# Optimization experiments

Measured on AMD Instinct MI355X. Metric: run time of the kernel, lower is better.

The kernel has to match this reference:

```python
import jax, jax.numpy as jnp
import numpy as np
from math import atanh

B, T, D_IN, H = 16, 1024, 512, 1024
INIT_A = atanh(0.95)


def setup_inputs() -> dict:
    key = jax.random.key(0)
    k1, k2, k3, k4 = jax.random.split(key, 4)
    x = jax.random.normal(k1, (B, T, D_IN), dtype=jnp.float32)
    h0 = jax.random.normal(k2, (B, H), dtype=jnp.float32)
    # raw_a initialized near atanh(0.95) as in the module, with small jitter
    raw_a = INIT_A + 0.01 * jax.random.normal(k3, (H,), dtype=jnp.float32)
    # xavier-uniform for W_x.weight [H, D_IN]
    limit = float(np.sqrt(6.0 / (D_IN + H)))
    W = jax.random.uniform(k4, (H, D_IN), dtype=jnp.float32, minval=-limit, maxval=limit)
    b = jnp.zeros((H,), dtype=jnp.float32)
    return {"x": x, "h0": h0, "raw_a": raw_a, "W": W, "b": b}


def reference(x, h0, raw_a, W, b):
    # h_t = a * h_{t-1} + W x_t + b, computed via cumprod/cumsum parallel-scan trick
    a = jnp.tanh(raw_a)                                   # [H] (rho is None)
    z = jnp.einsum('btd,hd->bth', x, W) + b               # [B,T,H]
    A = jnp.broadcast_to(a, (x.shape[1], a.shape[0]))     # [T,H]
    p = jnp.cumprod(A, axis=0)[None]                      # [1,T,H], p[t] = a^(t+1)
    v = jnp.cumsum(z / jnp.maximum(p, 1e-12), axis=1)     # [B,T,H]
    h = v * p + p * h0[:, None, :]                        # include initial state
    zero_mask = (jnp.abs(a) < 1e-6)[None, None, :]        # degenerate a ~ 0 channels
    h = jnp.where(zero_mask, z, h)
    return h
```

## Files before the change

kernel.cpp:

```cpp
#include <hip/hip_runtime.h>
#include <cstdint>

#define B_DIM 16
#define T_DIM 1024
#define DK    512
#define H_DIM 1024

typedef __bf16 bf16x8 __attribute__((ext_vector_type(8)));
typedef __bf16 bf16x4 __attribute__((ext_vector_type(4)));
typedef float  f32x4  __attribute__((ext_vector_type(4)));

typedef __attribute__((address_space(1))) unsigned int* as1p;
typedef __attribute__((address_space(3))) unsigned int* as3p;

__device__ __forceinline__ void async_cp16(const void* g, void* l) {
  __builtin_amdgcn_global_load_lds((as1p)(uint64_t)g,
                                   (as3p)(uint32_t)(uint64_t)l, 16, 0, 0);
}

__global__ __launch_bounds__(256) void cvt_f32_bf16(const float* __restrict__ in,
                                                    __bf16* __restrict__ out, int n4) {
  int i = blockIdx.x * 256 + threadIdx.x;
  if (i >= n4) return;
  f32x4 v = ((const f32x4*)in)[i];
  bf16x4 o;
  o.x = (__bf16)v.x; o.y = (__bf16)v.y; o.z = (__bf16)v.z; o.w = (__bf16)v.w;
  ((bf16x4*)out)[i] = o;
}

__global__ __launch_bounds__(256) void compute_meta(const float* __restrict__ raw_a,
                                                    float4* __restrict__ meta) {
  int h = blockIdx.x * 256 + threadIdx.x;
  if (h >= H_DIM) return;
  float a = tanhf(raw_a[h]);
  float la2 = log2f(fabsf(a));
  meta[h] = make_float4(a, la2, (a < 0.f) ? 1.f : 0.f, (fabsf(a) < 1e-6f) ? 1.f : 0.f);
}

__global__ __launch_bounds__(256, 2) void fused_rnn(const __bf16* __restrict__ xb,
                                                    const __bf16* __restrict__ wb,
                                                    const float* __restrict__ bias,
                                                    const float4* __restrict__ meta,
                                                    const float* __restrict__ h0g,
                                                    float* __restrict__ out) {
  __shared__ __align__(16) __bf16 As[2][2][256][32];
  __shared__ __align__(16) __bf16 Bs[2][2][32][32];
  __shared__ float chunkTot[4][32];
  __shared__ float colCarry[32];

  const int tid  = threadIdx.x;
  const int wave = tid >> 6;
  const int lane = tid & 63;
  const int q = lane >> 4;
  const int c = lane & 15;

  const int b  = blockIdx.x & 15;
  const int n0 = (blockIdx.x >> 4) * 32;

  float bias_j[2], la2_j[2], h0_j[2];
  bool neg_j[2], zm_j[2];
#pragma unroll
  for (int j = 0; j < 2; ++j) {
    const int col = n0 + j * 16 + c;
    bias_j[j] = bias[col];
    const float4 mt = meta[col];
    la2_j[j] = mt.y;
    neg_j[j] = mt.z != 0.f;
    zm_j[j]  = mt.w != 0.f;
    h0_j[j]  = h0g[(size_t)b * H_DIM + col];
  }

  if (tid < 32) colCarry[tid] = 0.f;

  const int srow = lane >> 2;
  const int skof = (lane & 3) * 8;

  const __bf16* const xbB = xb + (size_t)b * T_DIM * DK;

  auto stage = [&](int t0, int k0, int buf) {
#pragma unroll
    for (int h = 0; h < 2; ++h) {
#pragma unroll
      for (int r = 0; r < 4; ++r) {
        const int rg = wave * 64 + r * 16;
        const __bf16* ga = xbB + (size_t)(t0 + rg + srow) * DK + k0 + h * 32 + skof;
        async_cp16(ga, &As[buf][h][rg][0]);
      }
    }
    {
      const int h = wave >> 1, rp = (wave & 1) * 16;
      const __bf16* gb = wb + (size_t)(n0 + rp + srow) * DK + k0 + (wave >> 1) * 32 + skof;
      async_cp16(gb, &Bs[buf][h][rp][0]);
    }
  };

  stage(0, 0, 0);
  __syncthreads();

  for (int mc = 0; mc < 4; ++mc) {
    const int t0 = mc * 256;

    f32x4 acc[4][2];
#pragma unroll
    for (int i = 0; i < 4; ++i)
#pragma unroll
      for (int j = 0; j < 2; ++j) acc[i][j] = (f32x4){0.f, 0.f, 0.f, 0.f};

    for (int k = 0; k < 8; ++k) {
      const int buf = k & 1;
      if (k < 7)       stage(t0, (k + 1) * 64, buf ^ 1);
      else if (mc < 3) stage(t0 + 256, 0, 0);
#pragma unroll
      for (int ks = 0; ks < 2; ++ks) {
        bf16x8 af[4], bfr[2];
#pragma unroll
        for (int i = 0; i < 4; ++i)
          af[i] = *(const bf16x8*)(&As[buf][ks][wave * 64 + i * 16 + c][q * 8]);
#pragma unroll
        for (int j = 0; j < 2; ++j)
          bfr[j] = *(const bf16x8*)(&Bs[buf][ks][j * 16 + c][q * 8]);
#pragma unroll
        for (int i = 0; i < 4; ++i)
#pragma unroll
          for (int j = 0; j < 2; ++j)
            acc[i][j] = __builtin_amdgcn_mfma_f32_16x16x32_bf16(af[i], bfr[j], acc[i][j], 0, 0, 0);
      }
      __syncthreads();
    }

    f32x4 vloc[4][2];
    float icarry[2] = {0.f, 0.f};
#pragma unroll
    for (int i = 0; i < 4; ++i) {
#pragma unroll
      for (int j = 0; j < 2; ++j) {
        const float la2 = la2_j[j];
        f32x4 w;
#pragma unroll
        for (int r = 0; r < 4; ++r) {
          const int tp1 = t0 + wave * 64 + i * 16 + q * 4 + r + 1;
          const float z = acc[i][j][r] + bias_j[j];
          float inv = fminf(__builtin_amdgcn_exp2f(-la2 * (float)tp1), 1e12f);
          if (neg_j[j] && (tp1 & 1)) inv = 1e12f;
          w[r] = z * inv;
        }
        const float pr0 = w[0];
        const float pr1 = pr0 + w[1];
        const float pr2 = pr1 + w[2];
        const float pr3 = pr2 + w[3];
        const float x1 = __shfl_xor(pr3, 16, 64);
        const float x2 = __shfl_xor(pr3, 32, 64);
        const float x3 = __shfl_xor(pr3, 48, 64);
        float sq = 0.f;
        if (q >= 2) sq += x2 + x3;
        if (q & 1) sq += x1;
        const float base = icarry[j] + sq;
        vloc[i][j] = (f32x4){base + pr0, base + pr1, base + pr2, base + pr3};
        icarry[j] += pr3 + x1 + x2 + x3;
      }
    }
    if (q == 0) {
#pragma unroll
      for (int j = 0; j < 2; ++j) chunkTot[wave][j * 16 + c] = icarry[j];
    }
    __syncthreads();

    float cc[2];
#pragma unroll
    for (int j = 0; j < 2; ++j) {
      float s = colCarry[j * 16 + c];
      for (int w2 = 0; w2 < 4; ++w2)
        if (w2 < wave) s += chunkTot[w2][j * 16 + c];
      cc[j] = s;
    }
#pragma unroll
    for (int i = 0; i < 4; ++i) {
#pragma unroll
      for (int j = 0; j < 2; ++j) {
        const float la2 = la2_j[j];
        const int col = n0 + j * 16 + c;
#pragma unroll
        for (int r = 0; r < 4; ++r) {
          const int tl = t0 + wave * 64 + i * 16 + q * 4 + r;
          const int tp1 = tl + 1;
          float pv = __builtin_amdgcn_exp2f(la2 * (float)tp1);
          if (neg_j[j] && (tp1 & 1)) pv = -pv;
          const float v = cc[j] + vloc[i][j][r];
          const float hv = pv * v + pv * h0_j[j];
          const float zval = acc[i][j][r] + bias_j[j];
          out[(size_t)(b * T_DIM + tl) * H_DIM + col] = zm_j[j] ? zval : hv;
        }
      }
    }
    __syncthreads();
    if (tid < 32)
      colCarry[tid] += chunkTot[0][tid] + chunkTot[1][tid] + chunkTot[2][tid] + chunkTot[3][tid];
  }
}

extern "C" void kernel_launch(void* const* d_in, const int* in_sizes, int n_in,
                              void* d_out, int out_size, void* d_ws, size_t ws_size,
                              hipStream_t stream) {
  const float* x     = (const float*)d_in[0];
  const float* h0    = (const float*)d_in[1];
  const float* raw_a = (const float*)d_in[2];
  const float* W     = (const float*)d_in[3];
  const float* bias  = (const float*)d_in[4];
  float* out = (float*)d_out;

  char* ws = (char*)d_ws;
  __bf16* xb   = (__bf16*)(ws);
  __bf16* wb   = (__bf16*)(ws + 16777216);
  float4* meta = (float4*)(ws + 16777216 + 1048576);

  cvt_f32_bf16<<<(B_DIM * T_DIM * DK / 4 + 255) / 256, 256, 0, stream>>>(x, xb, B_DIM * T_DIM * DK / 4);
  cvt_f32_bf16<<<(H_DIM * DK / 4 + 255) / 256, 256, 0, stream>>>(W, wb, H_DIM * DK / 4);
  compute_meta<<<H_DIM / 256, 256, 0, stream>>>(raw_a, meta);
  fused_rnn<<<512, 256, 0, stream>>>(xb, wb, bias, meta, h0, out);
}
```

Measured before the change: 137.4 us.

## Split time into chunks across blocks with flag-based decoupled carry propagation

The fused kernel now splits the time axis into 128-step chunks handled by separate blocks. Each block has 512 threads and covers a 64-column strip, giving 2048 blocks instead of 512. Chunk carries pass between blocks through global flag words that are polled with atomics, replacing the serial in-block loop over four 256-step chunks. W is stored transposed and preloaded whole into LDS, while x is read straight from global memory into registers. The three prep kernels merge into one launch that also zeroes the flags. The cross-block spin-wait assumes earlier chunks get scheduled, which risks stalls or a deadlock if blocks run out of order.

```diff
diff --git a/kernel.cpp b/kernel.cpp
--- a/kernel.cpp
+++ b/kernel.cpp
@@ -6,6 +6,12 @@
 #define DK    512
 #define H_DIM 1024
 
+#define TCH    128
+#define NCH    (T_DIM / TCH)
+#define NB     64
+#define NSTRIP (H_DIM / NB)
+#define NKQ    (DK / 8)
+
 typedef __bf16 bf16x8 __attribute__((ext_vector_type(8)));
 typedef __bf16 bf16x4 __attribute__((ext_vector_type(4)));
 typedef float  f32x4  __attribute__((ext_vector_type(4)));
@@ -18,50 +24,79 @@
                                    (as3p)(uint32_t)(uint64_t)l, 16, 0, 0);
 }
 
-__global__ __launch_bounds__(256) void cvt_f32_bf16(const float* __restrict__ in,
-                                                    __bf16* __restrict__ out, int n4) {
-  int i = blockIdx.x * 256 + threadIdx.x;
-  if (i >= n4) return;
-  f32x4 v = ((const f32x4*)in)[i];
-  bf16x4 o;
-  o.x = (__bf16)v.x; o.y = (__bf16)v.y; o.z = (__bf16)v.z; o.w = (__bf16)v.w;
-  ((bf16x4*)out)[i] = o;
-}
-
-__global__ __launch_bounds__(256) void compute_meta(const float* __restrict__ raw_a,
-                                                    float4* __restrict__ meta) {
-  int h = blockIdx.x * 256 + threadIdx.x;
-  if (h >= H_DIM) return;
-  float a = tanhf(raw_a[h]);
-  float la2 = log2f(fabsf(a));
-  meta[h] = make_float4(a, la2, (a < 0.f) ? 1.f : 0.f, (fabsf(a) < 1e-6f) ? 1.f : 0.f);
-}
-
-__global__ __launch_bounds__(256, 2) void fused_rnn(const __bf16* __restrict__ xb,
-                                                    const __bf16* __restrict__ wb,
-                                                    const float* __restrict__ bias,
-                                                    const float4* __restrict__ meta,
-                                                    const float* __restrict__ h0g,
-                                                    float* __restrict__ out) {
-  __shared__ __align__(16) __bf16 As[2][2][256][32];
-  __shared__ __align__(16) __bf16 Bs[2][2][32][32];
-  __shared__ float chunkTot[4][32];
-  __shared__ float colCarry[32];
+__global__ __launch_bounds__(256) void prep(const float* __restrict__ x,
+                                            __bf16* __restrict__ xb,
+                                            const float* __restrict__ W,
+                                            __bf16* __restrict__ wbT,
+                                            const float* __restrict__ raw_a,
+                                            float4* __restrict__ meta,
+                                            unsigned long long* __restrict__ flags) {
+  const int bid = blockIdx.x, tid = threadIdx.x;
+  if (bid < 8192) {
+    const int i = bid * 256 + tid;
+    f32x4 v = ((const f32x4*)x)[i];
+    bf16x4 o;
+    o.x = (__bf16)v.x; o.y = (__bf16)v.y; o.z = (__bf16)v.z; o.w = (__bf16)v.w;
+    ((bf16x4*)xb)[i] = o;
+  } else if (bid < 8704) {
+    const int i = (bid - 8192) * 256 + tid;
+    const int h  = i >> 7;
+    const int k0 = (i & 127) * 4;
+    f32x4 v = ((const f32x4*)W)[i];
+    bf16x4 o;
+    o.x = (__bf16)v.x; o.y = (__bf16)v.y; o.z = (__bf16)v.z; o.w = (__bf16)v.w;
+    *(bf16x4*)(wbT + ((size_t)(k0 >> 3) * H_DIM + h) * 8 + (k0 & 7)) = o;
+  } else if (bid < 8708) {
+    const int h = (bid - 8704) * 256 + tid;
+    const float a = tanhf(raw_a[h]);
+    const float la2 = log2f(fabsf(a));
+    meta[h] = make_float4(a, la2, (a < 0.f) ? 1.f : 0.f, (fabsf(a) < 1e-6f) ? 1.f : 0.f);
+  } else {
+    const int i = (bid - 8708) * 256 + tid;
+    flags[i] = 0ULL;
+  }
+}
+
+__global__ __launch_bounds__(512, 4) void fused_rnn(
+    const __bf16* __restrict__ xb,
+    const __bf16* __restrict__ wbT,
+    const float* __restrict__ bias,
+    const float4* __restrict__ meta,
+    const float* __restrict__ h0g,
+    unsigned long long* __restrict__ flags,
+    float* __restrict__ out) {
+  __shared__ __align__(16) __bf16 Bs[NKQ][NB][8];
+  __shared__ float chunkTot[4][NB];
+  __shared__ float colCarry[NB];
 
   const int tid  = threadIdx.x;
   const int wave = tid >> 6;
   const int lane = tid & 63;
-  const int q = lane >> 4;
-  const int c = lane & 15;
-
-  const int b  = blockIdx.x & 15;
-  const int n0 = (blockIdx.x >> 4) * 32;
+  const int q  = lane >> 4;
+  const int c  = lane & 15;
+  const int rw = wave & 3;
+  const int cg = wave >> 2;
+
+  const int bid   = blockIdx.x;
+  const int g     = bid & 127;
+  const int strip = bid >> 7;
+  const int b     = g >> 3;
+  const int chunk = g & 7;
+  const int t0    = chunk * TCH;
+  const int n0    = strip * NB;
+
+#pragma unroll
+  for (int it = 0; it < 8; ++it) {
+    const int idx = it * 512 + tid;
+    const int col = idx & 63, kq = idx >> 6;
+    async_cp16(wbT + ((size_t)kq * H_DIM + (n0 + col)) * 8, &Bs[kq][col][0]);
+  }
 
   float bias_j[2], la2_j[2], h0_j[2];
   bool neg_j[2], zm_j[2];
 #pragma unroll
   for (int j = 0; j < 2; ++j) {
-    const int col = n0 + j * 16 + c;
+    const int col = n0 + cg * 32 + j * 16 + c;
     bias_j[j] = bias[col];
     const float4 mt = meta[col];
     la2_j[j] = mt.y;
@@ -70,131 +105,118 @@
     h0_j[j]  = h0g[(size_t)b * H_DIM + col];
   }
 
-  if (tid < 32) colCarry[tid] = 0.f;
-
-  const int srow = lane >> 2;
-  const int skof = (lane & 3) * 8;
-
-  const __bf16* const xbB = xb + (size_t)b * T_DIM * DK;
-
-  auto stage = [&](int t0, int k0, int buf) {
-#pragma unroll
-    for (int h = 0; h < 2; ++h) {
+  const __bf16* const arow =
+      xb + ((size_t)(b * T_DIM + t0 + rw * 32 + c)) * DK + q * 8;
+
+  f32x4 acc[2][2];
+#pragma unroll
+  for (int i = 0; i < 2; ++i)
+#pragma unroll
+    for (int j = 0; j < 2; ++j) acc[i][j] = (f32x4){0.f, 0.f, 0.f, 0.f};
+
+  __syncthreads();
+
+#pragma unroll 4
+  for (int k = 0; k < 16; ++k) {
+    bf16x8 af[2], bfr[2];
+#pragma unroll
+    for (int i = 0; i < 2; ++i)
+      af[i] = *(const bf16x8*)(arow + (size_t)i * 16 * DK + k * 32);
+#pragma unroll
+    for (int j = 0; j < 2; ++j)
+      bfr[j] = *(const bf16x8*)(&Bs[k * 4 + q][cg * 32 + j * 16 + c][0]);
+#pragma unroll
+    for (int i = 0; i < 2; ++i)
+#pragma unroll
+      for (int j = 0; j < 2; ++j)
+        acc[i][j] = __builtin_amdgcn_mfma_f32_16x16x32_bf16(af[i], bfr[j], acc[i][j], 0, 0, 0);
+  }
+
+  f32x4 vloc[2][2];
+  float icarry[2] = {0.f, 0.f};
+#pragma unroll
+  for (int i = 0; i < 2; ++i) {
+#pragma unroll
+    for (int j = 0; j < 2; ++j) {
+      const float la2 = la2_j[j];
+      f32x4 w;
 #pragma unroll
       for (int r = 0; r < 4; ++r) {
-        const int rg = wave * 64 + r * 16;
-        const __bf16* ga = xbB + (size_t)(t0 + rg + srow) * DK + k0 + h * 32 + skof;
-        async_cp16(ga, &As[buf][h][rg][0]);
+        const int tp1 = t0 + rw * 32 + i * 16 + q * 4 + r + 1;
+        const float z = acc[i][j][r] + bias_j[j];
+        float inv = fminf(__builtin_amdgcn_exp2f(-la2 * (float)tp1), 1e12f);
+        if (neg_j[j] && (tp1 & 1)) inv = 1e12f;
+        w[r] = z * inv;
+      }
+      const float pr0 = w[0];
+      const float pr1 = pr0 + w[1];
+      const float pr2 = pr1 + w[2];
+      const float pr3 = pr2 + w[3];
+      const float x1 = __shfl_xor(pr3, 16, 64);
+      const float x2 = __shfl_xor(pr3, 32, 64);
+      const float x3 = __shfl_xor(pr3, 48, 64);
+      float sq = 0.f;
+      if (q >= 2) sq += x2 + x3;
+      if (q & 1) sq += x1;
+      const float base = icarry[j] + sq;
+      vloc[i][j] = (f32x4){base + pr0, base + pr1, base + pr2, base + pr3};
+      icarry[j] += pr3 + x1 + x2 + x3;
+    }
+  }
+  if (q == 0) {
+#pragma unroll
+    for (int j = 0; j < 2; ++j) chunkTot[rw][cg * 32 + j * 16 + c] = icarry[j];
+  }
+  __syncthreads();
+
+  if (tid < 64) {
+    const int col = tid;
+    const size_t fb = ((size_t)b * NSTRIP + strip) * NCH * NB;
+    const float tot =
+        chunkTot[0][col] + chunkTot[1][col] + chunkTot[2][col] + chunkTot[3][col];
+    atomicExch(&flags[fb + (size_t)chunk * NB + col],
+               (1ULL << 32) | (unsigned long long)__float_as_uint(tot));
+    float s = 0.f;
+    for (int p = 0; p < chunk; ++p) {
+      unsigned long long v = atomicAdd(&flags[fb + (size_t)p * NB + col], 0ULL);
+      while (!(v >> 32)) {
+        __builtin_amdgcn_s_sleep(4);
+        v = atomicAdd(&flags[fb + (size_t)p * NB + col], 0ULL);
+      }
+      s += __uint_as_float((unsigned int)v);
+    }
+    colCarry[col] = s;
+  }
+  __syncthreads();
+
+  float cc[2];
+#pragma unroll
+  for (int j = 0; j < 2; ++j) {
+    const int colL = cg * 32 + j * 16 + c;
+    float s = colCarry[colL];
+#pragma unroll
+    for (int w2 = 0; w2 < 3; ++w2)
+      if (w2 < rw) s += chunkTot[w2][colL];
+    cc[j] = s;
+  }
+#pragma unroll
+  for (int i = 0; i < 2; ++i) {
+#pragma unroll
+    for (int j = 0; j < 2; ++j) {
+      const float la2 = la2_j[j];
+      const int col = n0 + cg * 32 + j * 16 + c;
+#pragma unroll
+      for (int r = 0; r < 4; ++r) {
+        const int tl = t0 + rw * 32 + i * 16 + q * 4 + r;
+        const int tp1 = tl + 1;
+        float pv = __builtin_amdgcn_exp2f(la2 * (float)tp1);
+        if (neg_j[j] && (tp1 & 1)) pv = -pv;
+        const float v = cc[j] + vloc[i][j][r];
+        const float hv = pv * v + pv * h0_j[j];
+        const float zval = acc[i][j][r] + bias_j[j];
+        out[(size_t)(b * T_DIM + tl) * H_DIM + col] = zm_j[j] ? zval : hv;
       }
     }
-    {
-      const int h = wave >> 1, rp = (wave & 1) * 16;
-      const __bf16* gb = wb + (size_t)(n0 + rp + srow) * DK + k0 + (wave >> 1) * 32 + skof;
-      async_cp16(gb, &Bs[buf][h][rp][0]);
-    }
-  };
-
-  stage(0, 0, 0);
-  __syncthreads();
-
-  for (int mc = 0; mc < 4; ++mc) {
-    const int t0 = mc * 256;
-
-    f32x4 acc[4][2];
-#pragma unroll
-    for (int i = 0; i < 4; ++i)
-#pragma unroll
-      for (int j = 0; j < 2; ++j) acc[i][j] = (f32x4){0.f, 0.f, 0.f, 0.f};
-
-    for (int k = 0; k < 8; ++k) {
-      const int buf = k & 1;
-      if (k < 7)       stage(t0, (k + 1) * 64, buf ^ 1);
-      else if (mc < 3) stage(t0 + 256, 0, 0);
-#pragma unroll
-      for (int ks = 0; ks < 2; ++ks) {
-        bf16x8 af[4], bfr[2];
-#pragma unroll
-        for (int i = 0; i < 4; ++i)
-          af[i] = *(const bf16x8*)(&As[buf][ks][wave * 64 + i * 16 + c][q * 8]);
-#pragma unroll
-        for (int j = 0; j < 2; ++j)
-          bfr[j] = *(const bf16x8*)(&Bs[buf][ks][j * 16 + c][q * 8]);
-#pragma unroll
-        for (int i = 0; i < 4; ++i)
-#pragma unroll
-          for (int j = 0; j < 2; ++j)
-            acc[i][j] = __builtin_amdgcn_mfma_f32_16x16x32_bf16(af[i], bfr[j], acc[i][j], 0, 0, 0);
-      }
-      __syncthreads();
-    }
-
-    f32x4 vloc[4][2];
-    float icarry[2] = {0.f, 0.f};
-#pragma unroll
-    for (int i = 0; i < 4; ++i) {
-#pragma unroll
-      for (int j = 0; j < 2; ++j) {
-        const float la2 = la2_j[j];
-        f32x4 w;
-#pragma unroll
-        for (int r = 0; r < 4; ++r) {
-          const int tp1 = t0 + wave * 64 + i * 16 + q * 4 + r + 1;
-          const float z = acc[i][j][r] + bias_j[j];
-          float inv = fminf(__builtin_amdgcn_exp2f(-la2 * (float)tp1), 1e12f);
-          if (neg_j[j] && (tp1 & 1)) inv = 1e12f;
-          w[r] = z * inv;
-        }
-        const float pr0 = w[0];
-        const float pr1 = pr0 + w[1];
-        const float pr2 = pr1 + w[2];
-        const float pr3 = pr2 + w[3];
-        const float x1 = __shfl_xor(pr3, 16, 64);
-        const float x2 = __shfl_xor(pr3, 32, 64);
-        const float x3 = __shfl_xor(pr3, 48, 64);
-        float sq = 0.f;
-        if (q >= 2) sq += x2 + x3;
-        if (q & 1) sq += x1;
-        const float base = icarry[j] + sq;
-        vloc[i][j] = (f32x4){base + pr0, base + pr1, base + pr2, base + pr3};
-        icarry[j] += pr3 + x1 + x2 + x3;
-      }
-    }
-    if (q == 0) {
-#pragma unroll
-      for (int j = 0; j < 2; ++j) chunkTot[wave][j * 16 + c] = icarry[j];
-    }
-    __syncthreads();
-
-    float cc[2];
-#pragma unroll
-    for (int j = 0; j < 2; ++j) {
-      float s = colCarry[j * 16 + c];
-      for (int w2 = 0; w2 < 4; ++w2)
-        if (w2 < wave) s += chunkTot[w2][j * 16 + c];
-      cc[j] = s;
-    }
-#pragma unroll
-    for (int i = 0; i < 4; ++i) {
-#pragma unroll
-      for (int j = 0; j < 2; ++j) {
-        const float la2 = la2_j[j];
-        const int col = n0 + j * 16 + c;
-#pragma unroll
-        for (int r = 0; r < 4; ++r) {
-          const int tl = t0 + wave * 64 + i * 16 + q * 4 + r;
-          const int tp1 = tl + 1;
-          float pv = __builtin_amdgcn_exp2f(la2 * (float)tp1);
-          if (neg_j[j] && (tp1 & 1)) pv = -pv;
-          const float v = cc[j] + vloc[i][j][r];
-          const float hv = pv * v + pv * h0_j[j];
-          const float zval = acc[i][j][r] + bias_j[j];
-          out[(size_t)(b * T_DIM + tl) * H_DIM + col] = zm_j[j] ? zval : hv;
-        }
-      }
-    }
-    __syncthreads();
-    if (tid < 32)
-      colCarry[tid] += chunkTot[0][tid] + chunkTot[1][tid] + chunkTot[2][tid] + chunkTot[3][tid];
   }
 }
 
@@ -209,12 +231,12 @@
   float* out = (float*)d_out;
 
   char* ws = (char*)d_ws;
-  __bf16* xb   = (__bf16*)(ws);
-  __bf16* wb   = (__bf16*)(ws + 16777216);
+  __bf16* xb  = (__bf16*)(ws);
+  __bf16* wbT = (__bf16*)(ws + 16777216);
   float4* meta = (float4*)(ws + 16777216 + 1048576);
-
-  cvt_f32_bf16<<<(B_DIM * T_DIM * DK / 4 + 255) / 256, 256, 0, stream>>>(x, xb, B_DIM * T_DIM * DK / 4);
-  cvt_f32_bf16<<<(H_DIM * DK / 4 + 255) / 256, 256, 0, stream>>>(W, wb, H_DIM * DK / 4);
-  compute_meta<<<H_DIM / 256, 256, 0, stream>>>(raw_a, meta);
-  fused_rnn<<<512, 256, 0, stream>>>(xb, wb, bias, meta, h0, out);
-}
+  unsigned long long* flags =
+      (unsigned long long*)(ws + 16777216 + 1048576 + 16384);
+
+  prep<<<9220, 256, 0, stream>>>(x, xb, W, wbT, raw_a, meta, flags);
+  fused_rnn<<<2048, 512, 0, stream>>>(xb, wbT, bias, meta, h0, flags, out);
+}
```

New measurement: 172.3 us. 1.25x slower.
